# Performance work log

Hardware: AMD Instinct MI355X
Metric: run time of the kernel (lower is better)

Reference implementation:

```python
import jax, jax.numpy as jnp
import numpy as np

B, N, EPG, FDIM, H = 128, 512, 4096, 128, 128
RATIO = 0.5
E = B * EPG
K1 = int(np.ceil(RATIO * N))      # 256
K2 = int(np.ceil(RATIO * K1))     # 128
K3 = int(np.ceil(RATIO * K2))     # 64


def setup_inputs():
    key = jax.random.key(0)
    ks = jax.random.split(key, 12)
    x = jax.random.normal(ks[0], (B * N, FDIM), jnp.float32)
    src = jax.random.randint(ks[1], (B, EPG), 0, N)
    dst = jax.random.randint(ks[2], (B, EPG), 0, N)
    off = (jnp.arange(B) * N)[:, None]
    edge_index = jnp.stack([(src + off).reshape(-1), (dst + off).reshape(-1)], 0).astype(jnp.int32)
    batch = (jnp.arange(B * N) // N).astype(jnp.int32)
    w = lambda k, s: jax.random.normal(k, s, jnp.float32) * 0.05
    return dict(
        x=x, edge_index=edge_index, batch=batch,
        W1=w(ks[3], (FDIM, H)), b1=jnp.zeros((H,), jnp.float32),
        Ws1=w(ks[4], (H, 1)), bs1=jnp.zeros((1,), jnp.float32),
        W2=w(ks[5], (H, H)), b2=jnp.zeros((H,), jnp.float32),
        Ws2=w(ks[6], (H, 1)), bs2=jnp.zeros((1,), jnp.float32),
        W3=w(ks[7], (H, H)), b3=jnp.zeros((H,), jnp.float32),
        Ws3=w(ks[8], (H, 1)), bs3=jnp.zeros((1,), jnp.float32))


def gcn(x, src, dst, emask, W, b):
    # PyG GCNConv: add self-loops, symmetric deg^-1/2 normalization.
    n = x.shape[0]
    h = x @ W
    deg = jnp.zeros((n,), x.dtype).at[dst].add(emask) + 1.0  # +1 for self-loop
    dinv = jax.lax.rsqrt(deg)
    norm = dinv[src] * dinv[dst] * emask                      # masked edges -> 0
    agg = jnp.zeros_like(h).at[dst].add(norm[:, None] * h[src])
    return agg + (dinv * dinv)[:, None] * h + b               # self-loop term + bias


def sag_pool(x, src, dst, emask, Ws, bs, n_per_graph, k):
    n_tot = x.shape[0]
    score = gcn(x, src, dst, emask, Ws, bs)[:, 0]
    sc = score.reshape(B, n_per_graph)
    topv, topi = jax.lax.top_k(sc, k)                         # [B,k] per-graph topk
    xg = x.reshape(B, n_per_graph, -1)
    xnew = jnp.take_along_axis(xg, topi[:, :, None], axis=1) * jnp.tanh(topv)[:, :, None]
    xnew = xnew.reshape(B * k, -1)
    perm = (topi + (jnp.arange(B) * n_per_graph)[:, None]).reshape(-1)
    newidx = jnp.full((n_tot,), -1, jnp.int32).at[perm].set(jnp.arange(B * k, dtype=jnp.int32))
    ns, nd = newidx[src], newidx[dst]
    valid = (ns >= 0) & (nd >= 0)
    emask_new = emask * valid.astype(x.dtype)                 # filter_adj via masking
    ns = jnp.where(valid, ns, 0)
    nd = jnp.where(valid, nd, 0)
    return xnew, ns, nd, emask_new


def readout(x, k):
    xg = x.reshape(B, k, -1)
    return jnp.concatenate([xg.max(axis=1), xg.mean(axis=1)], axis=1)  # [gmp, gap]


def reference(x, edge_index, batch, W1, b1, Ws1, bs1, W2, b2, Ws2, bs2, W3, b3, Ws3, bs3):
    src, dst = edge_index[0], edge_index[1]
    emask = jnp.ones((src.shape[0],), x.dtype)
    h = jax.nn.relu(gcn(x, src, dst, emask, W1, b1))
    h, src, dst, emask = sag_pool(h, src, dst, emask, Ws1, bs1, N, K1)
    x1 = readout(h, K1)
    h = jax.nn.relu(gcn(h, src, dst, emask, W2, b2))
    h, src, dst, emask = sag_pool(h, src, dst, emask, Ws2, bs2, K1, K2)
    x2 = readout(h, K2)
    h = jax.nn.relu(gcn(h, src, dst, emask, W3, b3))
    h, src, dst, emask = sag_pool(h, src, dst, emask, Ws3, bs3, K2, K3)
    x3 = readout(h, K3)
    return x1 + x2 + x3
```

## Files before the change

kernel.cpp:

```cpp
#include <hip/hip_runtime.h>
#include <math.h>

#define BGRAPH 128
#define ETOT   (128*4096)
#define EPG    4096
#define K1 256
#define K2 128
#define K3 64

__global__ __launch_bounds__(256) void gemm_tile3(const float* __restrict__ X,
                                                  const float* __restrict__ W,
                                                  float* __restrict__ Y){
  __shared__ float sA[128][33];
  __shared__ float sB[32][192];
  int t = threadIdx.x;
  int row0 = blockIdx.x * 128;
  int tx = t & 15;
  int ty = t >> 4;
  float acc[8][8];
  #pragma unroll
  for (int i = 0; i < 8; ++i)
    #pragma unroll
    for (int j = 0; j < 8; ++j) acc[i][j] = 0.f;

  for (int k0 = 0; k0 < 128; k0 += 32){
    #pragma unroll
    for (int i = 0; i < 4; ++i){
      int f = t + i*256;
      int row = f >> 3, c4 = f & 7;
      float4 v = *(const float4*)(X + (size_t)(row0 + row)*128 + k0 + c4*4);
      sA[row][c4*4+0] = v.x;
      sA[row][c4*4+1] = v.y;
      sA[row][c4*4+2] = v.z;
      sA[row][c4*4+3] = v.w;
    }
    #pragma unroll
    for (int i = 0; i < 4; ++i){
      int f = t + i*256;
      int kr = f >> 5, c4 = f & 31;
      int gg = c4 >> 1, hh = c4 & 1;
      float4 v = *(const float4*)(W + (size_t)(k0 + kr)*128 + c4*4);
      *(float4*)&sB[kr][gg*12 + hh*4] = v;
    }
    __syncthreads();
    #pragma unroll
    for (int kk = 0; kk < 32; ++kk){
      float4 b0 = *(const float4*)&sB[kk][tx*12];
      float4 b1 = *(const float4*)&sB[kk][tx*12 + 4];
      float aa[8];
      #pragma unroll
      for (int i = 0; i < 8; ++i) aa[i] = sA[ty*8 + i][kk];
      float bb[8] = {b0.x,b0.y,b0.z,b0.w,b1.x,b1.y,b1.z,b1.w};
      #pragma unroll
      for (int i = 0; i < 8; ++i)
        #pragma unroll
        for (int j = 0; j < 8; ++j)
          acc[i][j] = fmaf(aa[i], bb[j], acc[i][j]);
    }
    __syncthreads();
  }
  #pragma unroll
  for (int i = 0; i < 8; ++i){
    float* yr = Y + (size_t)(row0 + ty*8 + i)*128 + tx*8;
    *(float4*)yr       = *(float4*)&acc[i][0];
    *(float4*)(yr + 4) = *(float4*)&acc[i][4];
  }
}

__global__ __launch_bounds__(1024) void scanfill_l1(const int* __restrict__ src,
    const int* __restrict__ dst, int* __restrict__ off, int* __restrict__ cnt,
    float* __restrict__ dinv, int* __restrict__ csr, int* __restrict__ dsto,
    float* __restrict__ coef, int* __restrict__ ecnt){
  __shared__ int sc[512], sp[512], cur[512];
  __shared__ float sdv[512];
  __shared__ int ss[EPG], sd[EPG];
  int g = blockIdx.x, t = threadIdx.x;
  if (t < 512) sc[t] = 0;
  __syncthreads();
  const int* sg = src + g*EPG;
  const int* dg = dst + g*EPG;
  for (int e = t; e < EPG; e += 1024){
    int s = sg[e], d = dg[e];
    ss[e] = s; sd[e] = d;
    atomicAdd(&sc[d & 511], 1);
  }
  __syncthreads();
  int v = 0; float dv = 0.f;
  if (t < 512){
    v = sc[t];
    dv = rsqrtf((float)v + 1.f);
    sdv[t] = dv;
    dinv[g*512 + t] = dv;
    cnt[g*512 + t] = v;
    sp[t] = v;
  }
  __syncthreads();
  for (int d = 1; d < 512; d <<= 1){
    int u = 0;
    if (t >= d && t < 512) u = sp[t-d];
    __syncthreads();
    if (t < 512) sp[t] += u;
    __syncthreads();
  }
  if (t < 512){
    int pre = sp[t] - v;
    off[g*512 + t] = g*EPG + pre;
    sc[t] = pre;
    cur[t] = 0;
  }
  if (t == 0) ecnt[g] = EPG;
  __syncthreads();
  int* cg = csr + g*EPG;
  int* dg2 = dsto + g*EPG;
  float* cf = coef + g*EPG;
  for (int e = t; e < EPG; e += 1024){
    int s = ss[e], dl = sd[e] & 511;
    int slot = sc[dl] + atomicAdd(&cur[dl], 1);
    cg[slot]  = s;
    dg2[slot] = g*512 + dl;
    cf[slot]  = sdv[s & 511] * sdv[dl];
  }
}

__global__ void gather_agg(const float* __restrict__ hx, const int* __restrict__ csr,
                           const float* __restrict__ coef,
                           const int* __restrict__ off, const int* __restrict__ cnt,
                           const float* __restrict__ dinv, const float* __restrict__ bias,
                           const float* __restrict__ Ws, float* __restrict__ out,
                           float* __restrict__ hs, int npg, int n){
  int bpg = npg >> 3;
  int x = blockIdx.x >> 3, r = blockIdx.x & 7;
  int pos = x % bpg, grp = x / bpg;
  int g = grp*8 + r;
  int t = threadIdx.x;
  int node = g*npg + pos*8 + (t >> 5);
  int fl = t & 31;
  float dd = dinv[node];
  int o = off[node], deg = cnt[node];
  const float4* rows = (const float4*)hx;
  float4 a0 = {0,0,0,0}, a1 = {0,0,0,0}, a2 = {0,0,0,0}, a3 = {0,0,0,0};
  int e = o, end = o + deg;
  for (; e + 7 < end; e += 8){
    int sx[8]; float cx[8]; float4 vv[8];
    #pragma unroll
    for (int q = 0; q < 8; ++q){ sx[q] = csr[e+q]; cx[q] = coef[e+q]; }
    #pragma unroll
    for (int q = 0; q < 8; ++q) vv[q] = rows[(size_t)sx[q]*32 + fl];
    #pragma unroll
    for (int q = 0; q < 8; ++q){
      float4& aq = (q&3)==0 ? a0 : ((q&3)==1 ? a1 : ((q&3)==2 ? a2 : a3));
      aq.x = fmaf(cx[q], vv[q].x, aq.x);
      aq.y = fmaf(cx[q], vv[q].y, aq.y);
      aq.z = fmaf(cx[q], vv[q].z, aq.z);
      aq.w = fmaf(cx[q], vv[q].w, aq.w);
    }
  }
  for (; e + 3 < end; e += 4){
    int sx[4]; float cx[4]; float4 vv[4];
    #pragma unroll
    for (int q = 0; q < 4; ++q){ sx[q] = csr[e+q]; cx[q] = coef[e+q]; }
    #pragma unroll
    for (int q = 0; q < 4; ++q) vv[q] = rows[(size_t)sx[q]*32 + fl];
    #pragma unroll
    for (int q = 0; q < 4; ++q){
      float4& aq = (q==0) ? a0 : ((q==1) ? a1 : ((q==2) ? a2 : a3));
      aq.x = fmaf(cx[q], vv[q].x, aq.x);
      aq.y = fmaf(cx[q], vv[q].y, aq.y);
      aq.z = fmaf(cx[q], vv[q].z, aq.z);
      aq.w = fmaf(cx[q], vv[q].w, aq.w);
    }
  }
  for (; e < end; ++e){
    int s0 = csr[e];
    float c0 = coef[e];
    float4 v0 = rows[(size_t)s0*32 + fl];
    a0.x=fmaf(c0,v0.x,a0.x); a0.y=fmaf(c0,v0.y,a0.y); a0.z=fmaf(c0,v0.z,a0.z); a0.w=fmaf(c0,v0.w,a0.w);
  }
  float4 own = rows[(size_t)node*32 + fl];
  float4 bv  = ((const float4*)bias)[fl];
  float d2 = dd*dd;
  float4 rr;
  rr.x = fmaxf(fmaf(d2, own.x, (a0.x+a1.x)+(a2.x+a3.x) + bv.x), 0.f);
  rr.y = fmaxf(fmaf(d2, own.y, (a0.y+a1.y)+(a2.y+a3.y) + bv.y), 0.f);
  rr.z = fmaxf(fmaf(d2, own.z, (a0.z+a1.z)+(a2.z+a3.z) + bv.z), 0.f);
  rr.w = fmaxf(fmaf(d2, own.w, (a0.w+a1.w)+(a2.w+a3.w) + bv.w), 0.f);
  ((float4*)(out + (size_t)node*128))[fl] = rr;
  float4 w = ((const float4*)Ws)[fl];
  float p = rr.x*w.x + rr.y*w.y + rr.z*w.z + rr.w*w.w;
  p += __shfl_xor(p, 16);
  p += __shfl_xor(p, 8);
  p += __shfl_xor(p, 4);
  p += __shfl_xor(p, 2);
  p += __shfl_xor(p, 1);
  if (fl == 0) hs[node] = p;
}

template<int NP, int K, int HASNEXT, int FIRST>
__global__ __launch_bounds__(1024) void mega(
    const float* __restrict__ hs, const int* __restrict__ csr_in,
    const int* __restrict__ dst_in, const float* __restrict__ coef_in,
    const int* __restrict__ off_in, const int* __restrict__ cnt_in,
    const float* __restrict__ dinv_in, const float* __restrict__ bs,
    const float* __restrict__ Hm, float* __restrict__ xnew, float* __restrict__ out,
    const int* __restrict__ ecnt_in,
    int* __restrict__ off_o, int* __restrict__ cnt_o, float* __restrict__ dinv_o,
    int* __restrict__ csr_o, int* __restrict__ dst_o, float* __restrict__ coef_o,
    int* __restrict__ ecnt_o)
{
  constexpr int R   = 1024 / NP;
  constexpr int LNP = (NP == 512) ? 9 : ((NP == 256) ? 8 : 7);
  __shared__ int   ss[EPG];
  __shared__ int   sd[EPG];
  __shared__ float scf[EPG];
  __shared__ float shs[NP];
  __shared__ float spart[1024];
  __shared__ float sv[NP];
  __shared__ int   si[NP];
  __shared__ int   lnew[NP];
  __shared__ int   lperm[K];
  __shared__ float ltanh[K];
  __shared__ float smx[1024], ssm[1024];
  __shared__ int   sc[K], sp2[K], cur[K];
  __shared__ float sdvn[K];
  int g = blockIdx.x, t = threadIdx.x;
  int E_in = ecnt_in[g];

  if (t < NP){ shs[t] = hs[g*NP + t]; lnew[t] = -1; }
  for (int e = t; e < E_in; e += 1024){
    ss[e]  = csr_in[g*EPG + e];
    sd[e]  = dst_in[g*EPG + e];
    scf[e] = coef_in[g*EPG + e];
  }
  __syncthreads();

  int n = t & (NP-1);
  int p = t >> LNP;
  {
    int lo = off_in[g*NP + n] - g*EPG, deg = cnt_in[g*NP + n];
    float a = 0.f;
    for (int e = lo + p; e < lo + deg; e += R)
      a = fmaf(scf[e], shs[ss[e] & (NP-1)], a);
    spart[t] = a;
  }
  __syncthreads();
  float v = -INFINITY; int idx = n;
  if (p == 0){
    float a = spart[n];
    #pragma unroll
    for (int q = 1; q < R; ++q) a += spart[n + q*NP];
    float dd = dinv_in[g*NP + n];
    v = a + fmaf(dd*dd, shs[n], bs[0]);
  }
  #pragma unroll
  for (int ksz = 2; ksz <= NP; ksz <<= 1){
    #pragma unroll
    for (int j = ksz >> 1; j > 0; j >>= 1){
      float v2 = 0.f; int i2 = 0;
      if (j >= 64){
        __syncthreads();
        if (t < NP){ sv[t] = v; si[t] = idx; }
        __syncthreads();
        if (t < NP){ v2 = sv[t^j]; i2 = si[t^j]; }
      } else if (t < NP){
        v2 = __shfl_xor(v, j);
        i2 = __shfl_xor(idx, j);
      }
      if (t < NP){
        bool dir = ((t & ksz) == 0);
        bool pf = (v2 > v) || (v2 == v && i2 < idx);
        bool lower = (t & j) == 0;
        if (pf == (lower ? dir : !dir)){ v = v2; idx = i2; }
      }
    }
  }
  if (t < K){
    lperm[t] = idx;
    lnew[idx] = t;
    ltanh[t] = tanhf(v);
  }
  __syncthreads();

  {
    int f = t & 127, q = t >> 7;
    float mx = -INFINITY, sm = 0.f;
    for (int j = q; j < K; j += 8){
      float val = Hm[(size_t)(g*NP + lperm[j])*128 + f] * ltanh[j];
      xnew[(size_t)(g*K + j)*128 + f] = val;
      mx = fmaxf(mx, val); sm += val;
    }
    smx[t] = mx; ssm[t] = sm;
  }
  __syncthreads();
  if (t < 128){
    float mx = smx[t], sm = ssm[t];
    #pragma unroll
    for (int q = 1; q < 8; ++q){ mx = fmaxf(mx, smx[q*128+t]); sm += ssm[q*128+t]; }
    if (FIRST){
      out[g*256 + t]       = mx;
      out[g*256 + 128 + t] = sm / (float)K;
    } else {
      out[g*256 + t]       += mx;
      out[g*256 + 128 + t] += sm / (float)K;
    }
  }
  if (!HASNEXT) return;
  __syncthreads();

  if (t < K) sc[t] = 0;
  __syncthreads();
  for (int e = t; e < E_in; e += 1024){
    int rs = lnew[ss[e] & (NP-1)], rd = lnew[sd[e] & (NP-1)];
    bool ok = (rs | rd) >= 0;
    ss[e] = rs;
    sd[e] = ok ? rd : -1;
    if (ok) atomicAdd(&sc[rd], 1);
  }
  __syncthreads();
  int cv = 0; float dvn = 0.f;
  if (t < K){
    cv = sc[t];
    dvn = rsqrtf((float)cv + 1.f);
    sdvn[t] = dvn;
    dinv_o[g*K + t] = dvn;
    cnt_o[g*K + t] = cv;
    sp2[t] = cv;
  }
  __syncthreads();
  for (int d = 1; d < K; d <<= 1){
    int u = 0;
    if (t >= d && t < K) u = sp2[t-d];
    __syncthreads();
    if (t < K) sp2[t] += u;
    __syncthreads();
  }
  if (t < K){
    int pre = sp2[t] - cv;
    off_o[g*K + t] = g*EPG + pre;
    sc[t] = pre;
    cur[t] = 0;
    if (t == K-1) ecnt_o[g] = pre + cv;
  }
  __syncthreads();
  for (int e = t; e < E_in; e += 1024){
    int ndl = sd[e];
    if (ndl < 0) continue;
    int nsl = ss[e];
    int slot = sc[ndl] + atomicAdd(&cur[ndl], 1);
    csr_o[g*EPG + slot]  = g*K + nsl;
    dst_o[g*EPG + slot]  = g*K + ndl;
    coef_o[g*EPG + slot] = sdvn[nsl] * sdvn[ndl];
  }
}

extern "C" void kernel_launch(void* const* d_in, const int* in_sizes, int n_in,
                              void* d_out, int out_size, void* d_ws, size_t ws_size,
                              hipStream_t stream){
  const float* x0 = (const float*)d_in[0];
  const int*   ei = (const int*)d_in[1];
  const float* Wl[3]  = {(const float*)d_in[3], (const float*)d_in[7],  (const float*)d_in[11]};
  const float* bl[3]  = {(const float*)d_in[4], (const float*)d_in[8],  (const float*)d_in[12]};
  const float* Wsl[3] = {(const float*)d_in[5], (const float*)d_in[9],  (const float*)d_in[13]};
  const float* bsl[3] = {(const float*)d_in[6], (const float*)d_in[10], (const float*)d_in[14]};

  float* A     = (float*)d_ws;
  float* C     = A + (size_t)65536*128;
  float* D     = C + (size_t)65536*128;
  float* dinvA = D + (size_t)32768*128;
  float* dinvB = dinvA + 65536;
  float* hs    = dinvB + 65536;
  int* cntA    = (int*)(hs + 65536);
  int* cntB    = cntA + 65536;
  int* offA    = cntB + 65536;
  int* offB    = offA + 65536;
  int* csrA    = offB + 65536;
  int* csrB    = csrA + ETOT;
  int* dstA    = csrB + ETOT;
  int* dstB    = dstA + ETOT;
  float* coefA = (float*)(dstB + ETOT);
  float* coefB = coefA + ETOT;
  int* ecntA   = (int*)(coefB + ETOT);
  int* ecntB   = ecntA + 128;

  float* out = (float*)d_out;

  scanfill_l1<<<BGRAPH, 1024, 0, stream>>>(ei, ei + ETOT, offA, cntA, dinvA, csrA, dstA, coefA, ecntA);
  gemm_tile3<<<65536/128, 256, 0, stream>>>(x0, Wl[0], A);
  gather_agg<<<65536/8, 256, 0, stream>>>(A, csrA, coefA, offA, cntA, dinvA, bl[0], Wsl[0], C, hs, 512, 65536);
  mega<512, K1, 1, 1><<<BGRAPH, 1024, 0, stream>>>(hs, csrA, dstA, coefA, offA, cntA, dinvA, bsl[0],
      C, D, out, ecntA, offB, cntB, dinvB, csrB, dstB, coefB, ecntB);
  gemm_tile3<<<32768/128, 256, 0, stream>>>(D, Wl[1], A);
  gather_agg<<<32768/8, 256, 0, stream>>>(A, csrB, coefB, offB, cntB, dinvB, bl[1], Wsl[1], C, hs, 256, 32768);
  mega<256, K2, 1, 0><<<BGRAPH, 1024, 0, stream>>>(hs, csrB, dstB, coefB, offB, cntB, dinvB, bsl[1],
      C, D, out, ecntB, offA, cntA, dinvA, csrA, dstA, coefA, ecntA);
  gemm_tile3<<<16384/128, 256, 0, stream>>>(D, Wl[2], A);
  gather_agg<<<16384/8, 256, 0, stream>>>(A, csrA, coefA, offA, cntA, dinvA, bl[2], Wsl[2], C, hs, 128, 16384);
  mega<128, K3, 0, 0><<<BGRAPH, 1024, 0, stream>>>(hs, csrA, dstA, coefA, offA, cntA, dinvA, bsl[2],
      C, D, out, ecntA, offB, cntB, dinvB, csrB, dstB, coefB, ecntB);
}
```

Measured before the change: 189.7 us.

## Pad CSR rows to multiples of eight and read edges directly from global

```diff
diff --git a/kernel.cpp b/kernel.cpp
--- a/kernel.cpp
+++ b/kernel.cpp
@@ -4,6 +4,7 @@
 #define BGRAPH 128
 #define ETOT   (128*4096)
 #define EPG    4096
+#define ES     8192
 #define K1 256
 #define K2 128
 #define K3 64
@@ -85,14 +86,15 @@
     atomicAdd(&sc[d & 511], 1);
   }
   __syncthreads();
-  int v = 0; float dv = 0.f;
+  int v = 0, pv = 0; float dv = 0.f;
   if (t < 512){
     v = sc[t];
+    pv = (v + 7) & ~7;
     dv = rsqrtf((float)v + 1.f);
     sdv[t] = dv;
     dinv[g*512 + t] = dv;
-    cnt[g*512 + t] = v;
-    sp[t] = v;
+    cnt[g*512 + t] = pv;
+    sp[t] = pv;
   }
   __syncthreads();
   for (int d = 1; d < 512; d <<= 1){
@@ -102,17 +104,22 @@
     if (t < 512) sp[t] += u;
     __syncthreads();
   }
+  int* cg = csr + g*ES;
+  int* dg2 = dsto + g*ES;
+  float* cf = coef + g*ES;
   if (t < 512){
-    int pre = sp[t] - v;
-    off[g*512 + t] = g*EPG + pre;
+    int pre = sp[t] - pv;
+    off[g*512 + t] = g*ES + pre;
     sc[t] = pre;
     cur[t] = 0;
-  }
-  if (t == 0) ecnt[g] = EPG;
-  __syncthreads();
-  int* cg = csr + g*EPG;
-  int* dg2 = dsto + g*EPG;
-  float* cf = coef + g*EPG;
+    if (t == 511) ecnt[g] = sp[511];
+    for (int e = v; e < pv; ++e){
+      cg[pre + e]  = 0;
+      dg2[pre + e] = -1;
+      cf[pre + e]  = 0.f;
+    }
+  }
+  __syncthreads();
   for (int e = t; e < EPG; e += 1024){
     int s = ss[e], dl = sd[e] & 511;
     int slot = sc[dl] + atomicAdd(&cur[dl], 1);
@@ -139,42 +146,27 @@
   int o = off[node], deg = cnt[node];
   const float4* rows = (const float4*)hx;
   float4 a0 = {0,0,0,0}, a1 = {0,0,0,0}, a2 = {0,0,0,0}, a3 = {0,0,0,0};
-  int e = o, end = o + deg;
-  for (; e + 7 < end; e += 8){
-    int sx[8]; float cx[8]; float4 vv[8];
-    #pragma unroll
-    for (int q = 0; q < 8; ++q){ sx[q] = csr[e+q]; cx[q] = coef[e+q]; }
-    #pragma unroll
-    for (int q = 0; q < 8; ++q) vv[q] = rows[(size_t)sx[q]*32 + fl];
-    #pragma unroll
-    for (int q = 0; q < 8; ++q){
-      float4& aq = (q&3)==0 ? a0 : ((q&3)==1 ? a1 : ((q&3)==2 ? a2 : a3));
-      aq.x = fmaf(cx[q], vv[q].x, aq.x);
-      aq.y = fmaf(cx[q], vv[q].y, aq.y);
-      aq.z = fmaf(cx[q], vv[q].z, aq.z);
-      aq.w = fmaf(cx[q], vv[q].w, aq.w);
-    }
-  }
-  for (; e + 3 < end; e += 4){
-    int sx[4]; float cx[4]; float4 vv[4];
-    #pragma unroll
-    for (int q = 0; q < 4; ++q){ sx[q] = csr[e+q]; cx[q] = coef[e+q]; }
-    #pragma unroll
-    for (int q = 0; q < 4; ++q) vv[q] = rows[(size_t)sx[q]*32 + fl];
-    #pragma unroll
-    for (int q = 0; q < 4; ++q){
-      float4& aq = (q==0) ? a0 : ((q==1) ? a1 : ((q==2) ? a2 : a3));
-      aq.x = fmaf(cx[q], vv[q].x, aq.x);
-      aq.y = fmaf(cx[q], vv[q].y, aq.y);
-      aq.z = fmaf(cx[q], vv[q].z, aq.z);
-      aq.w = fmaf(cx[q], vv[q].w, aq.w);
-    }
-  }
-  for (; e < end; ++e){
-    int s0 = csr[e];
-    float c0 = coef[e];
-    float4 v0 = rows[(size_t)s0*32 + fl];
-    a0.x=fmaf(c0,v0.x,a0.x); a0.y=fmaf(c0,v0.y,a0.y); a0.z=fmaf(c0,v0.z,a0.z); a0.w=fmaf(c0,v0.w,a0.w);
+  for (int e = o; e < o + deg; e += 8){
+    int4   i0 = *(const int4*)(csr + e);
+    int4   i1 = *(const int4*)(csr + e + 4);
+    float4 c0 = *(const float4*)(coef + e);
+    float4 c1 = *(const float4*)(coef + e + 4);
+    float4 v0 = rows[(size_t)i0.x*32 + fl];
+    float4 v1 = rows[(size_t)i0.y*32 + fl];
+    float4 v2 = rows[(size_t)i0.z*32 + fl];
+    float4 v3 = rows[(size_t)i0.w*32 + fl];
+    float4 v4 = rows[(size_t)i1.x*32 + fl];
+    float4 v5 = rows[(size_t)i1.y*32 + fl];
+    float4 v6 = rows[(size_t)i1.z*32 + fl];
+    float4 v7 = rows[(size_t)i1.w*32 + fl];
+    a0.x=fmaf(c0.x,v0.x,a0.x); a0.y=fmaf(c0.x,v0.y,a0.y); a0.z=fmaf(c0.x,v0.z,a0.z); a0.w=fmaf(c0.x,v0.w,a0.w);
+    a1.x=fmaf(c0.y,v1.x,a1.x); a1.y=fmaf(c0.y,v1.y,a1.y); a1.z=fmaf(c0.y,v1.z,a1.z); a1.w=fmaf(c0.y,v1.w,a1.w);
+    a2.x=fmaf(c0.z,v2.x,a2.x); a2.y=fmaf(c0.z,v2.y,a2.y); a2.z=fmaf(c0.z,v2.z,a2.z); a2.w=fmaf(c0.z,v2.w,a2.w);
+    a3.x=fmaf(c0.w,v3.x,a3.x); a3.y=fmaf(c0.w,v3.y,a3.y); a3.z=fmaf(c0.w,v3.z,a3.z); a3.w=fmaf(c0.w,v3.w,a3.w);
+    a0.x=fmaf(c1.x,v4.x,a0.x); a0.y=fmaf(c1.x,v4.y,a0.y); a0.z=fmaf(c1.x,v4.z,a0.z); a0.w=fmaf(c1.x,v4.w,a0.w);
+    a1.x=fmaf(c1.y,v5.x,a1.x); a1.y=fmaf(c1.y,v5.y,a1.y); a1.z=fmaf(c1.y,v5.z,a1.z); a1.w=fmaf(c1.y,v5.w,a1.w);
+    a2.x=fmaf(c1.z,v6.x,a2.x); a2.y=fmaf(c1.z,v6.y,a2.y); a2.z=fmaf(c1.z,v6.z,a2.z); a2.w=fmaf(c1.z,v6.w,a2.w);
+    a3.x=fmaf(c1.w,v7.x,a3.x); a3.y=fmaf(c1.w,v7.y,a3.y); a3.z=fmaf(c1.w,v7.z,a3.z); a3.w=fmaf(c1.w,v7.w,a3.w);
   }
   float4 own = rows[(size_t)node*32 + fl];
   float4 bv  = ((const float4*)bias)[fl];
@@ -209,9 +201,6 @@
 {
   constexpr int R   = 1024 / NP;
   constexpr int LNP = (NP == 512) ? 9 : ((NP == 256) ? 8 : 7);
-  __shared__ int   ss[EPG];
-  __shared__ int   sd[EPG];
-  __shared__ float scf[EPG];
   __shared__ float shs[NP];
   __shared__ float spart[1024];
   __shared__ float sv[NP];
@@ -226,20 +215,15 @@
   int E_in = ecnt_in[g];
 
   if (t < NP){ shs[t] = hs[g*NP + t]; lnew[t] = -1; }
-  for (int e = t; e < E_in; e += 1024){
-    ss[e]  = csr_in[g*EPG + e];
-    sd[e]  = dst_in[g*EPG + e];
-    scf[e] = coef_in[g*EPG + e];
-  }
   __syncthreads();
 
   int n = t & (NP-1);
   int p = t >> LNP;
   {
-    int lo = off_in[g*NP + n] - g*EPG, deg = cnt_in[g*NP + n];
+    int lo = off_in[g*NP + n], deg = cnt_in[g*NP + n];
     float a = 0.f;
     for (int e = lo + p; e < lo + deg; e += R)
-      a = fmaf(scf[e], shs[ss[e] & (NP-1)], a);
+      a = fmaf(coef_in[e], shs[csr_in[e] & (NP-1)], a);
     spart[t] = a;
   }
   __syncthreads();
@@ -309,21 +293,22 @@
   if (t < K) sc[t] = 0;
   __syncthreads();
   for (int e = t; e < E_in; e += 1024){
-    int rs = lnew[ss[e] & (NP-1)], rd = lnew[sd[e] & (NP-1)];
-    bool ok = (rs | rd) >= 0;
-    ss[e] = rs;
-    sd[e] = ok ? rd : -1;
-    if (ok) atomicAdd(&sc[rd], 1);
-  }
-  __syncthreads();
-  int cv = 0; float dvn = 0.f;
+    int d = dst_in[g*ES + e];
+    if (d < 0) continue;
+    int rs = lnew[csr_in[g*ES + e] & (NP-1)];
+    int rd = lnew[d & (NP-1)];
+    if ((rs | rd) >= 0) atomicAdd(&sc[rd], 1);
+  }
+  __syncthreads();
+  int cv = 0, pcv = 0; float dvn = 0.f;
   if (t < K){
     cv = sc[t];
+    pcv = (cv + 7) & ~7;
     dvn = rsqrtf((float)cv + 1.f);
     sdvn[t] = dvn;
     dinv_o[g*K + t] = dvn;
-    cnt_o[g*K + t] = cv;
-    sp2[t] = cv;
+    cnt_o[g*K + t] = pcv;
+    sp2[t] = pcv;
   }
   __syncthreads();
   for (int d = 1; d < K; d <<= 1){
@@ -334,21 +319,28 @@
     __syncthreads();
   }
   if (t < K){
-    int pre = sp2[t] - cv;
-    off_o[g*K + t] = g*EPG + pre;
+    int pre = sp2[t] - pcv;
+    off_o[g*K + t] = g*ES + pre;
     sc[t] = pre;
     cur[t] = 0;
-    if (t == K-1) ecnt_o[g] = pre + cv;
+    if (t == K-1) ecnt_o[g] = sp2[K-1];
+    for (int e = cv; e < pcv; ++e){
+      csr_o[g*ES + pre + e]  = g*K;
+      dst_o[g*ES + pre + e]  = -1;
+      coef_o[g*ES + pre + e] = 0.f;
+    }
   }
   __syncthreads();
   for (int e = t; e < E_in; e += 1024){
-    int ndl = sd[e];
-    if (ndl < 0) continue;
-    int nsl = ss[e];
-    int slot = sc[ndl] + atomicAdd(&cur[ndl], 1);
-    csr_o[g*EPG + slot]  = g*K + nsl;
-    dst_o[g*EPG + slot]  = g*K + ndl;
-    coef_o[g*EPG + slot] = sdvn[nsl] * sdvn[ndl];
+    int d = dst_in[g*ES + e];
+    if (d < 0) continue;
+    int rs = lnew[csr_in[g*ES + e] & (NP-1)];
+    int rd = lnew[d & (NP-1)];
+    if ((rs | rd) < 0) continue;
+    int slot = sc[rd] + atomicAdd(&cur[rd], 1);
+    csr_o[g*ES + slot]  = g*K + rs;
+    dst_o[g*ES + slot]  = g*K + rd;
+    coef_o[g*ES + slot] = sdvn[rs] * sdvn[rd];
   }
 }
 
@@ -373,12 +365,12 @@
   int* offA    = cntB + 65536;
   int* offB    = offA + 65536;
   int* csrA    = offB + 65536;
-  int* csrB    = csrA + ETOT;
-  int* dstA    = csrB + ETOT;
-  int* dstB    = dstA + ETOT;
-  float* coefA = (float*)(dstB + ETOT);
-  float* coefB = coefA + ETOT;
-  int* ecntA   = (int*)(coefB + ETOT);
+  int* csrB    = csrA + 128*ES;
+  int* dstA    = csrB + 128*ES;
+  int* dstB    = dstA + 128*ES;
+  float* coefA = (float*)(dstB + 128*ES);
+  float* coefB = coefA + 128*ES;
+  int* ecntA   = (int*)(coefB + 128*ES);
   int* ecntB   = ecntA + 128;
 
   float* out = (float*)d_out;
```

Measured after the change: 201.6 us. 6.3% more time.

## Fuse layer-1 CSR build and first GEMM into one block-specialized launch

Applied to the files above, without the earlier changes.

```diff
diff --git a/kernel.cpp b/kernel.cpp
--- a/kernel.cpp
+++ b/kernel.cpp
@@ -67,58 +67,119 @@
   }
 }
 
-__global__ __launch_bounds__(1024) void scanfill_l1(const int* __restrict__ src,
-    const int* __restrict__ dst, int* __restrict__ off, int* __restrict__ cnt,
-    float* __restrict__ dinv, int* __restrict__ csr, int* __restrict__ dsto,
-    float* __restrict__ coef, int* __restrict__ ecnt){
-  __shared__ int sc[512], sp[512], cur[512];
-  __shared__ float sdv[512];
-  __shared__ int ss[EPG], sd[EPG];
-  int g = blockIdx.x, t = threadIdx.x;
-  if (t < 512) sc[t] = 0;
-  __syncthreads();
-  const int* sg = src + g*EPG;
-  const int* dg = dst + g*EPG;
-  for (int e = t; e < EPG; e += 1024){
-    int s = sg[e], d = dg[e];
-    ss[e] = s; sd[e] = d;
-    atomicAdd(&sc[d & 511], 1);
-  }
-  __syncthreads();
-  int v = 0; float dv = 0.f;
-  if (t < 512){
-    v = sc[t];
-    dv = rsqrtf((float)v + 1.f);
-    sdv[t] = dv;
-    dinv[g*512 + t] = dv;
-    cnt[g*512 + t] = v;
-    sp[t] = v;
-  }
-  __syncthreads();
-  for (int d = 1; d < 512; d <<= 1){
-    int u = 0;
-    if (t >= d && t < 512) u = sp[t-d];
-    __syncthreads();
-    if (t < 512) sp[t] += u;
-    __syncthreads();
-  }
-  if (t < 512){
-    int pre = sp[t] - v;
-    off[g*512 + t] = g*EPG + pre;
-    sc[t] = pre;
-    cur[t] = 0;
-  }
-  if (t == 0) ecnt[g] = EPG;
-  __syncthreads();
-  int* cg = csr + g*EPG;
-  int* dg2 = dsto + g*EPG;
-  float* cf = coef + g*EPG;
-  for (int e = t; e < EPG; e += 1024){
-    int s = ss[e], dl = sd[e] & 511;
-    int slot = sc[dl] + atomicAdd(&cur[dl], 1);
-    cg[slot]  = s;
-    dg2[slot] = g*512 + dl;
-    cf[slot]  = sdv[s & 511] * sdv[dl];
+__global__ __launch_bounds__(256) void fused_l1(const float* __restrict__ X,
+    const float* __restrict__ W, float* __restrict__ Y,
+    const int* __restrict__ src, const int* __restrict__ dst,
+    int* __restrict__ off, int* __restrict__ cnt, float* __restrict__ dinv,
+    int* __restrict__ csr, int* __restrict__ dsto, float* __restrict__ coef,
+    int* __restrict__ ecnt){
+  extern __shared__ float smem[];
+  int t = threadIdx.x;
+  if (blockIdx.x < 512){
+    float* sA = smem;
+    float* sB = smem + 128*33;
+    int row0 = blockIdx.x * 128;
+    int tx = t & 15;
+    int ty = t >> 4;
+    float acc[8][8];
+    #pragma unroll
+    for (int i = 0; i < 8; ++i)
+      #pragma unroll
+      for (int j = 0; j < 8; ++j) acc[i][j] = 0.f;
+
+    for (int k0 = 0; k0 < 128; k0 += 32){
+      #pragma unroll
+      for (int i = 0; i < 4; ++i){
+        int f = t + i*256;
+        int row = f >> 3, c4 = f & 7;
+        float4 v = *(const float4*)(X + (size_t)(row0 + row)*128 + k0 + c4*4);
+        sA[row*33 + c4*4+0] = v.x;
+        sA[row*33 + c4*4+1] = v.y;
+        sA[row*33 + c4*4+2] = v.z;
+        sA[row*33 + c4*4+3] = v.w;
+      }
+      #pragma unroll
+      for (int i = 0; i < 4; ++i){
+        int f = t + i*256;
+        int kr = f >> 5, c4 = f & 31;
+        int gg = c4 >> 1, hh = c4 & 1;
+        float4 v = *(const float4*)(W + (size_t)(k0 + kr)*128 + c4*4);
+        *(float4*)&sB[kr*192 + gg*12 + hh*4] = v;
+      }
+      __syncthreads();
+      #pragma unroll
+      for (int kk = 0; kk < 32; ++kk){
+        float4 b0 = *(const float4*)&sB[kk*192 + tx*12];
+        float4 b1 = *(const float4*)&sB[kk*192 + tx*12 + 4];
+        float aa[8];
+        #pragma unroll
+        for (int i = 0; i < 8; ++i) aa[i] = sA[(ty*8 + i)*33 + kk];
+        float bb[8] = {b0.x,b0.y,b0.z,b0.w,b1.x,b1.y,b1.z,b1.w};
+        #pragma unroll
+        for (int i = 0; i < 8; ++i)
+          #pragma unroll
+          for (int j = 0; j < 8; ++j)
+            acc[i][j] = fmaf(aa[i], bb[j], acc[i][j]);
+      }
+      __syncthreads();
+    }
+    #pragma unroll
+    for (int i = 0; i < 8; ++i){
+      float* yr = Y + (size_t)(row0 + ty*8 + i)*128 + tx*8;
+      *(float4*)yr       = *(float4*)&acc[i][0];
+      *(float4*)(yr + 4) = *(float4*)&acc[i][4];
+    }
+  } else {
+    int g = blockIdx.x - 512;
+    int*   sc  = (int*)smem;
+    int*   sp  = sc + 512;
+    int*   cur = sp + 256;
+    float* sdv = (float*)(cur + 512);
+    int*   ss  = (int*)(sdv + 512);
+    int*   sd  = ss + 4096;
+    sc[t] = 0; sc[t + 256] = 0;
+    __syncthreads();
+    const int* sg = src + g*EPG;
+    const int* dg = dst + g*EPG;
+    for (int e = t; e < EPG; e += 256){
+      int s = sg[e], d = dg[e];
+      ss[e] = s; sd[e] = d;
+      atomicAdd(&sc[d & 511], 1);
+    }
+    __syncthreads();
+    int a = sc[2*t], b = sc[2*t+1];
+    int pair = a + b;
+    sp[t] = pair;
+    __syncthreads();
+    for (int d = 1; d < 256; d <<= 1){
+      int u = (t >= d) ? sp[t-d] : 0;
+      __syncthreads();
+      sp[t] += u;
+      __syncthreads();
+    }
+    int pre0 = sp[t] - pair;
+    int pre1 = pre0 + a;
+    float dv0 = rsqrtf((float)a + 1.f);
+    float dv1 = rsqrtf((float)b + 1.f);
+    sdv[2*t]   = dv0;  sdv[2*t+1] = dv1;
+    dinv[g*512 + 2*t]   = dv0;  dinv[g*512 + 2*t+1] = dv1;
+    cnt[g*512 + 2*t]    = a;    cnt[g*512 + 2*t+1]  = b;
+    off[g*512 + 2*t]    = g*EPG + pre0;
+    off[g*512 + 2*t+1]  = g*EPG + pre1;
+    sc[2*t] = pre0; sc[2*t+1] = pre1;
+    cur[2*t] = 0;   cur[2*t+1] = 0;
+    if (t == 0) ecnt[g] = EPG;
+    __syncthreads();
+    int* cg = csr + g*EPG;
+    int* dg2 = dsto + g*EPG;
+    float* cf = coef + g*EPG;
+    for (int e = t; e < EPG; e += 256){
+      int s = ss[e], dl = sd[e] & 511;
+      int slot = sc[dl] + atomicAdd(&cur[dl], 1);
+      cg[slot]  = s;
+      dg2[slot] = g*512 + dl;
+      cf[slot]  = sdv[s & 511] * sdv[dl];
+    }
   }
 }
 
@@ -383,8 +444,9 @@
 
   float* out = (float*)d_out;
 
-  scanfill_l1<<<BGRAPH, 1024, 0, stream>>>(ei, ei + ETOT, offA, cntA, dinvA, csrA, dstA, coefA, ecntA);
-  gemm_tile3<<<65536/128, 256, 0, stream>>>(x0, Wl[0], A);
+  size_t shbytes = (size_t)(128*33 + 32*192) * sizeof(float);
+  fused_l1<<<640, 256, shbytes, stream>>>(x0, Wl[0], A,
+      ei, ei + ETOT, offA, cntA, dinvA, csrA, dstA, coefA, ecntA);
   gather_agg<<<65536/8, 256, 0, stream>>>(A, csrA, coefA, offA, cntA, dinvA, bl[0], Wsl[0], C, hs, 512, 65536);
   mega<512, K1, 1, 1><<<BGRAPH, 1024, 0, stream>>>(hs, csrA, dstA, coefA, offA, cntA, dinvA, bsl[0],
       C, D, out, ecntA, offB, cntB, dinvB, csrB, dstB, coefB, ecntB);
```

After: 183.0 us. 3.5% less time.
